# Optimization experiments

Measured on AMD Instinct MI355X. Metric: run time of the kernel, lower is better.

The kernel has to match this reference:

```python
import jax, jax.numpy as jnp
import numpy as np

NUM_EMBEDDINGS = 1024
EMBED_DIM = 256
EMA_DECAY = 0.99
EPS = 1e-05


def setup_inputs() -> dict:
    key = jax.random.key(0)
    k1, k2, k3 = jax.random.split(key, 3)
    B, D, H, W = 32, EMBED_DIM, 32, 32
    z = jax.random.normal(k1, (B, D, H, W), dtype=jnp.float32)
    # torch init: uniform(-1/K, 1/K)
    scale = 1.0 / NUM_EMBEDDINGS
    embedding = jax.random.uniform(k2, (NUM_EMBEDDINGS, EMBED_DIM), dtype=jnp.float32,
                                   minval=-scale, maxval=scale)
    ema_cluster_size = jnp.zeros((NUM_EMBEDDINGS,), dtype=jnp.float32)
    # buffer initialized to a copy of the embedding weights
    ema_embed_sum = embedding.copy()
    return {"z": z, "embedding": embedding,
            "ema_cluster_size": ema_cluster_size, "ema_embed_sum": ema_embed_sum}


def reference(z, embedding, ema_cluster_size, ema_embed_sum):
    B, D, H, W = z.shape
    K = embedding.shape[0]
    # (B, D, H, W) -> (N, D) with N = B*H*W
    z_flat = jnp.transpose(z, (0, 2, 3, 1)).reshape(-1, D)
    # squared L2 distances: ||z||^2 - 2 z E^T + ||e||^2  -> (N, K)
    distances = (jnp.sum(z_flat * z_flat, axis=1, keepdims=True)
                 - 2.0 * z_flat @ embedding.T
                 + jnp.sum(embedding * embedding, axis=1)[None, :])
    indices = jnp.argmin(distances, axis=1)  # (N,) int32
    z_q = embedding[indices].reshape(B, H, W, D).transpose(0, 3, 1, 2)  # (B, D, H, W)

    # training-mode EMA updates (pure functional: return new buffers / codebook)
    ones = jnp.ones((z_flat.shape[0],), dtype=z_flat.dtype)
    counts = jax.ops.segment_sum(ones, indices, num_segments=K)          # (K,)
    embed_sum = jax.ops.segment_sum(z_flat, indices, num_segments=K)     # (K, D)
    new_cs = EMA_DECAY * ema_cluster_size + (1.0 - EMA_DECAY) * counts
    new_es = EMA_DECAY * ema_embed_sum + (1.0 - EMA_DECAY) * embed_sum
    n = jnp.sum(new_cs)
    cluster_size = (new_cs + EPS) / (n + K * EPS) * n
    new_embedding = new_es / cluster_size[:, None]

    # commitment loss and straight-through estimator
    commitment_loss = jnp.mean((z - jax.lax.stop_gradient(z_q)) ** 2)
    z_q_st = z + jax.lax.stop_gradient(z_q - z)
    indices_grid = indices.reshape(B, H, W)
    return (z_q_st, commitment_loss, indices_grid, new_embedding, new_cs, new_es)
```

## Files before the change

### kernel.cpp

```cpp
#include <hip/hip_runtime.h>

#define D_  256
#define K_  1024
#define HW_ 1024
#define N_  32768

#define WS_COUNTS  262144
#define WS_EMBSUM  266240
#define WS_LOSS    1314816
#define WS_NSUM    1314820
#define WS_ENORM   1318924
#define WS_E16     1454096
#define WS_TOTAL   1978384

#define O_ZQ   0
#define O_LOSS 8388608
#define O_IDX  8388609
#define O_EMB  8421377
#define O_NCS  8683521
#define O_NES  8684545

typedef unsigned short u16;
typedef _Float16 f16x8 __attribute__((ext_vector_type(8)));
typedef float f32x4 __attribute__((ext_vector_type(4)));

__device__ __forceinline__ unsigned f16x2pack(float a, float b) {
  union { _Float16 h; unsigned short u; } ca, cb;
  ca.h = (_Float16)a; cb.h = (_Float16)b;
  return (unsigned)ca.u | ((unsigned)cb.u << 16);
}

__device__ __forceinline__ float pw256_sq(const float* __restrict__ p, int stride) {
  float tot0 = 0.f, tot1 = 0.f;
#pragma unroll
  for (int h = 0; h < 2; ++h) {
    const float* q = p + h * 128 * stride;
    float r[8];
#pragma unroll
    for (int j = 0; j < 8; ++j) { float x = q[j * stride]; r[j] = __fmul_rn(x, x); }
    for (int i = 8; i < 128; i += 8)
#pragma unroll
      for (int j = 0; j < 8; ++j) {
        float x = q[(i + j) * stride];
        r[j] = __fadd_rn(r[j], __fmul_rn(x, x));
      }
    float s = __fadd_rn(__fadd_rn(__fadd_rn(r[0], r[1]), __fadd_rn(r[2], r[3])),
                        __fadd_rn(__fadd_rn(r[4], r[5]), __fadd_rn(r[6], r[7])));
    if (h == 0) tot0 = s; else tot1 = s;
  }
  return __fadd_rn(tot0, tot1);
}

__global__ void vq_eprep(const float* __restrict__ E, float* __restrict__ enorm,
                         u16* __restrict__ E16, float* __restrict__ zero0) {
  int gid = blockIdx.x * 256 + threadIdx.x;
  if (gid < K_) {
    float v = pw256_sq(E + gid * D_, 1);
    enorm[gid] = v;
  }
  unsigned* E16w = (unsigned*)E16;
  for (int wd = gid; wd < (K_ * D_ / 2); wd += 8192) {
    float2 x = *(const float2*)(E + 2 * wd);
    E16w[wd] = f16x2pack(512.0f * x.x, 512.0f * x.y);
  }
  float4 z4 = {0.f, 0.f, 0.f, 0.f};
  float4* zp = (float4*)zero0;
  for (int i = gid; i < 65792; i += 8192) zp[i] = z4;
  if (gid == 0) { zero0[263168] = 0.f; zero0[263169] = 0.f; }
}

template <int CTRL>
__device__ __forceinline__ float dppmin(float v) {
  int p = __builtin_amdgcn_update_dpp(0, __float_as_int(v), CTRL, 0xF, 0xF, true);
  return fminf(v, __int_as_float(p));
}

__device__ __forceinline__ void exact_update(
    const float* zrow, const float* __restrict__ E, int t, int c,
    const float* zn_s, const float* en_s, unsigned long long* best_s) {
  const float* ep = E + c * D_;
  float a = 0.f;
  for (int d0 = 0; d0 < 256; d0 += 8) {
    f32x4 z0 = *(const f32x4*)(zrow + d0);
    f32x4 z1 = *(const f32x4*)(zrow + d0 + 4);
    float4 e0 = *(const float4*)(ep + d0);
    float4 e1 = *(const float4*)(ep + d0 + 4);
    a = __fmaf_rn(z0[0], e0.x, a); a = __fmaf_rn(z0[1], e0.y, a);
    a = __fmaf_rn(z0[2], e0.z, a); a = __fmaf_rn(z0[3], e0.w, a);
    a = __fmaf_rn(z1[0], e1.x, a); a = __fmaf_rn(z1[1], e1.y, a);
    a = __fmaf_rn(z1[2], e1.z, a); a = __fmaf_rn(z1[3], e1.w, a);
  }
  float s = __fadd_rn(__fsub_rn(zn_s[t], __fmul_rn(2.0f, a)), en_s[c]);
  unsigned long long key = ((unsigned long long)__float_as_uint(s) << 32) | (unsigned)c;
  atomicMin(&best_s[t], key);
}

#define TCAP 96
#define ZP  260

__global__ __launch_bounds__(256, 4) void vq_main(
    const float* __restrict__ z, const float* __restrict__ E,
    const u16* __restrict__ E16, const float* __restrict__ enorm,
    float* __restrict__ embsum, float* __restrict__ loss_sum,
    float* __restrict__ counts, float* __restrict__ out_zq,
    float* __restrict__ out_idx) {
  __shared__ __align__(16) float zs[32 * ZP];
  __shared__ float en_s[K_];
  __shared__ float zn_s[32];
  __shared__ float mg_s[32];
  __shared__ unsigned rmin_s[32];
  __shared__ unsigned long long best_s[32];
  __shared__ unsigned tcount[4];
  __shared__ unsigned tlist[4][TCAP];
  __shared__ float wred[4];

  const int tid = threadIdx.x;
  const int tile = blockIdx.x;
  const int bimg = tile >> 5;
  const int hw0 = (tile & 31) << 5;
  const float* zb = z + bimg * (D_ * HW_) + hw0;
  const int n0 = bimg * HW_ + hw0;

#pragma unroll
  for (int r = 0; r < 8; ++r) {
    int ii = r * 256 + tid;
    int d = ii >> 3, t4 = (ii & 7) * 4;
    float4 v = *(const float4*)(zb + d * HW_ + t4);
    zs[(t4 + 0) * ZP + d] = v.x; zs[(t4 + 1) * ZP + d] = v.y;
    zs[(t4 + 2) * ZP + d] = v.z; zs[(t4 + 3) * ZP + d] = v.w;
  }
  {
    float emx = 0.f;
    for (int i = tid; i < K_; i += 256) {
      float v = enorm[i];
      en_s[i] = v;
      emx = fmaxf(emx, v);
    }
#pragma unroll
    for (int o = 32; o > 0; o >>= 1) emx = fmaxf(emx, __shfl_down(emx, o, 64));
    if ((tid & 63) == 0) wred[tid >> 6] = emx;
  }
  if (tid < 4) tcount[tid] = 0;
  __syncthreads();
  if (tid < 32) {
    float zn = pw256_sq(&zs[tid * ZP], 1);
    zn_s[tid] = zn;
    float em = fmaxf(fmaxf(wred[0], wred[1]), fmaxf(wred[2], wred[3]));
    mg_s[tid] = 0.00390625f * sqrtf(zn * em) + 5e-4f;
    rmin_s[tid] = 0xFFFFFFFFu;
    best_s[tid] = ~0ull;
  }
  __syncthreads();

  const int lane = tid & 63;
  const int w = tid >> 6;
  const int l15 = lane & 15, g = lane >> 4;
  const int cw = w * 256;
  const u16* Eb = E16 + (unsigned)(cw + l15) * D_ + g * 8;

  f16x8 efA[2], efB[2];
#pragma unroll
  for (int n = 0; n < 2; ++n)
    efA[n] = *(const f16x8*)(Eb + n * 16 * D_);

  f32x4 acc[2][2];

#define MSTEP(S, EFU, EFF, SN)                                                   \
  {                                                                              \
    const int kk_ = (S) & 7;                                                     \
    {                                                                            \
      const int cn_ = (SN) >> 3, kn_ = (SN) & 7;                                 \
      _Pragma("unroll")                                                          \
      for (int n = 0; n < 2; ++n)                                                \
        EFF[n] = *(const f16x8*)(Eb + (cn_ * 32 + n * 16) * D_ + kn_ * 32);      \
    }                                                                            \
    f16x8 zf_[2];                                                                \
    _Pragma("unroll")                                                            \
    for (int m = 0; m < 2; ++m) {                                                \
      const float* zr = zs + (m * 16 + l15) * ZP + kk_ * 32 + g * 8;             \
      f32x4 lo = *(const f32x4*)zr;                                              \
      f32x4 hi = *(const f32x4*)(zr + 4);                                        \
      f16x8 zc;                                                                  \
      _Pragma("unroll")                                                          \
      for (int j = 0; j < 4; ++j) {                                              \
        zc[j] = (_Float16)lo[j]; zc[4 + j] = (_Float16)hi[j];                    \
      }                                                                          \
      zf_[m] = zc;                                                               \
    }                                                                            \
    _Pragma("unroll")                                                            \
    for (int m = 0; m < 2; ++m)                                                  \
      _Pragma("unroll")                                                          \
      for (int n = 0; n < 2; ++n)                                                \
        acc[m][n] = __builtin_amdgcn_mfma_f32_16x16x32_f16(zf_[m], EFU[n],       \
                                                           acc[m][n], 0, 0, 0);  \
  }

  for (int s2 = 0; s2 < 64; s2 += 2) {
    if ((s2 & 7) == 0) {
      f32x4 z4 = {0.f, 0.f, 0.f, 0.f};
#pragma unroll
      for (int m = 0; m < 2; ++m)
#pragma unroll
        for (int n = 0; n < 2; ++n) acc[m][n] = z4;
    }
    MSTEP(s2, efA, efB, s2 + 1)
    MSTEP(s2 + 1, efB, efA, (s2 + 2) & 63)
    if ((s2 & 7) == 6) {
      const int cb = cw + (s2 >> 3) * 32;
      float enc[2];
#pragma unroll
      for (int n = 0; n < 2; ++n) enc[n] = en_s[cb + n * 16 + l15];
#pragma unroll
      for (int m = 0; m < 2; ++m)
#pragma unroll
        for (int n = 0; n < 2; ++n)
#pragma unroll
          for (int r = 0; r < 4; ++r)
            acc[m][n][r] = __builtin_fmaf(-0.00390625f, acc[m][n][r], enc[n]);
#pragma unroll
      for (int m = 0; m < 2; ++m)
#pragma unroll
        for (int r = 0; r < 4; ++r) {
          float v = fminf(acc[m][0][r], acc[m][1][r]);
          v = dppmin<0xB1>(v);
          v = dppmin<0x4E>(v);
          v = dppmin<0x141>(v);
          v = dppmin<0x140>(v);
          if (l15 == 0) atomicMin(&rmin_s[m * 16 + g * 4 + r], __float_as_uint(v + 4.0f));
        }
#pragma unroll
      for (int m = 0; m < 2; ++m)
#pragma unroll
        for (int r = 0; r < 4; ++r) {
          int t = m * 16 + g * 4 + r;
          float thr = (__uint_as_float(rmin_s[t]) - 4.0f) + mg_s[t];
#pragma unroll
          for (int n = 0; n < 2; ++n) {
            if (acc[m][n][r] <= thr) {
              unsigned pos = atomicAdd(&tcount[w], 1u);
              if (pos < TCAP)
                tlist[w][pos] = ((unsigned)t << 16) | (unsigned)(cb + n * 16 + l15);
            }
          }
        }
    }
  }
#undef MSTEP

  {
    unsigned cnt = tcount[w];
    if (cnt <= TCAP) {
      for (unsigned basei = 0; basei < cnt; basei += 64) {
        unsigned i = basei + (unsigned)lane;
        if (i < cnt) {
          unsigned e = tlist[w][i];
          int t = (int)(e >> 16), c = (int)(e & 1023u);
          exact_update(&zs[t * ZP], E, t, c, zn_s, en_s, best_s);
        }
      }
    } else {
      for (unsigned i = (unsigned)lane; i < 32u * 256u; i += 64) {
        int t = (int)(i >> 8), c = cw + (int)(i & 255u);
        exact_update(&zs[t * ZP], E, t, c, zn_s, en_s, best_s);
      }
    }
  }
  __syncthreads();

  if (tid < 32) {
    int k = (int)(best_s[tid] & 1023ull);
    out_idx[n0 + tid] = (float)k;
    atomicAdd(&counts[k], 1.0f);
  }
  float lsum = 0.f;
  for (int tt = 0; tt < 8; ++tt) {
    int t = w * 8 + tt;
    int k = (int)(best_s[t] & 1023ull);
    const float* Er = E + k * D_;
    float* es = embsum + k * D_;
#pragma unroll
    for (int i = 0; i < 4; ++i) {
      int d = i * 64 + lane;
      float e = Er[d];
      float zv = zs[t * ZP + d];
      float df = __fsub_rn(zv, e);
      lsum += df * df;
      zs[t * ZP + d] = __fadd_rn(zv, __fsub_rn(e, zv));
      atomicAdd(es + d, zv);
    }
  }
#pragma unroll
  for (int o = 32; o > 0; o >>= 1) lsum += __shfl_down(lsum, o, 64);
  if (lane == 0) wred[w] = lsum;
  __syncthreads();
  if (tid == 0) atomicAdd(loss_sum, wred[0] + wred[1] + wred[2] + wred[3]);

  float* ob = out_zq + bimg * (D_ * HW_) + hw0;
#pragma unroll 4
  for (int r = 0; r < 32; ++r) {
    int d = r * 8 + (tid >> 5);
    int t = tid & 31;
    ob[d * HW_ + t] = zs[t * ZP + d];
  }
}

__global__ void vq_newfin(const float* __restrict__ cs_in, const float* __restrict__ counts,
                          const float* __restrict__ es_in, const float* __restrict__ embsum,
                          const float* __restrict__ loss_sum,
                          float* __restrict__ out_loss, float* __restrict__ out_ncs,
                          float* __restrict__ out_emb, float* __restrict__ out_nes) {
  __shared__ float nred[4];
  const int k = blockIdx.x, d = threadIdx.x;
  float s = 0.f;
  float myv[4];
#pragma unroll
  for (int i = 0; i < 4; ++i) {
    int idx = i * 256 + d;
    float v = __fadd_rn(__fmul_rn(0.99f, cs_in[idx]), __fmul_rn(0.01f, counts[idx]));
    myv[i] = v;
    s += v;
  }
#pragma unroll
  for (int o = 32; o > 0; o >>= 1) s += __shfl_down(s, o, 64);
  if ((d & 63) == 0) nred[d >> 6] = s;
  __syncthreads();
  const float n = (nred[0] + nred[1]) + (nred[2] + nred[3]);
  if (d == (k & 255)) out_ncs[k] = myv[k >> 8];
  if (k == 0 && d == 0) out_loss[0] = loss_sum[0] * (1.0f / 8388608.0f);
  float vk = __fadd_rn(__fmul_rn(0.99f, cs_in[k]), __fmul_rn(0.01f, counts[k]));
  float cs = (vk + 1e-5f) / (n + 1024.0f * 1e-5f) * n;
  float es = __fadd_rn(__fmul_rn(0.99f, es_in[k * D_ + d]),
                       __fmul_rn(0.01f, embsum[k * D_ + d]));
  out_nes[k * D_ + d] = es;
  out_emb[k * D_ + d] = es / cs;
}

extern "C" void kernel_launch(void* const* d_in, const int* in_sizes, int n_in,
                              void* d_out, int out_size, void* d_ws, size_t ws_size,
                              hipStream_t stream) {
  (void)in_sizes; (void)n_in; (void)out_size; (void)ws_size;
  const float* z       = (const float*)d_in[0];
  const float* E       = (const float*)d_in[1];
  const float* ema_cs  = (const float*)d_in[2];
  const float* ema_es  = (const float*)d_in[3];
  float* out = (float*)d_out;
  char* ws = (char*)d_ws;
  float* counts = (float*)(ws + WS_COUNTS);
  float* embsum = (float*)(ws + WS_EMBSUM);
  float* loss_s = (float*)(ws + WS_LOSS);
  float* enorm  = (float*)(ws + WS_ENORM);
  u16*   e16    = (u16*)(ws + WS_E16);

  vq_eprep<<<dim3(32), dim3(256), 0, stream>>>(E, enorm, e16, counts);
  vq_main<<<dim3(1024), dim3(256), 0, stream>>>(z, E, e16, enorm,
                                                embsum, loss_s, counts,
                                                out + O_ZQ, out + O_IDX);
  vq_newfin<<<dim3(K_), dim3(256), 0, stream>>>(ema_cs, counts, ema_es, embsum,
                                                loss_s, out + O_LOSS, out + O_NCS,
                                                out + O_EMB, out + O_NES);
}
```

Measured before the change: 209.5 us.

## Pre-pack z tile to f16 in LDS and read enorm from global

The main kernel now builds a pre-converted f16 copy of the z tile in shared memory, laid out to match the MFMA operand fragments. Each step then does one vector LDS load per fragment instead of two fp32 loads plus eight conversions. The shared copy of the codebook norms is dropped and reads go straight to global/L2, which frees LDS for the new buffer. The prep kernel launches 256 blocks instead of 32 so the E16 conversion and the workspace zeroing run wider. The cost is an extra strided global read of z to build the f16 tile, plus global loads of enorm inside the hot loop.

```diff
diff --git a/kernel.cpp b/kernel.cpp
--- a/kernel.cpp
+++ b/kernel.cpp
@@ -59,13 +59,13 @@
     enorm[gid] = v;
   }
   unsigned* E16w = (unsigned*)E16;
-  for (int wd = gid; wd < (K_ * D_ / 2); wd += 8192) {
+  for (int wd = gid; wd < (K_ * D_ / 2); wd += 65536) {
     float2 x = *(const float2*)(E + 2 * wd);
     E16w[wd] = f16x2pack(512.0f * x.x, 512.0f * x.y);
   }
   float4 z4 = {0.f, 0.f, 0.f, 0.f};
   float4* zp = (float4*)zero0;
-  for (int i = gid; i < 65792; i += 8192) zp[i] = z4;
+  for (int i = gid; i < 65792; i += 65536) zp[i] = z4;
   if (gid == 0) { zero0[263168] = 0.f; zero0[263169] = 0.f; }
 }
 
@@ -77,7 +77,7 @@
 
 __device__ __forceinline__ void exact_update(
     const float* zrow, const float* __restrict__ E, int t, int c,
-    const float* zn_s, const float* en_s, unsigned long long* best_s) {
+    const float* zn_s, const float* __restrict__ en, unsigned long long* best_s) {
   const float* ep = E + c * D_;
   float a = 0.f;
   for (int d0 = 0; d0 < 256; d0 += 8) {
@@ -90,7 +90,7 @@
     a = __fmaf_rn(z1[0], e1.x, a); a = __fmaf_rn(z1[1], e1.y, a);
     a = __fmaf_rn(z1[2], e1.z, a); a = __fmaf_rn(z1[3], e1.w, a);
   }
-  float s = __fadd_rn(__fsub_rn(zn_s[t], __fmul_rn(2.0f, a)), en_s[c]);
+  float s = __fadd_rn(__fsub_rn(zn_s[t], __fmul_rn(2.0f, a)), en[c]);
   unsigned long long key = ((unsigned long long)__float_as_uint(s) << 32) | (unsigned)c;
   atomicMin(&best_s[t], key);
 }
@@ -105,7 +105,7 @@
     float* __restrict__ counts, float* __restrict__ out_zq,
     float* __restrict__ out_idx) {
   __shared__ __align__(16) float zs[32 * ZP];
-  __shared__ float en_s[K_];
+  __shared__ __align__(16) u16 zt16[32 * 32 * 8];
   __shared__ float zn_s[32];
   __shared__ float mg_s[32];
   __shared__ unsigned rmin_s[32];
@@ -130,12 +130,24 @@
     zs[(t4 + 2) * ZP + d] = v.z; zs[(t4 + 3) * ZP + d] = v.w;
   }
   {
+    const int tok = tid & 31;
+    const int kbase = (tid >> 5) * 4;
+    for (int r = 0; r < 4; ++r) {
+      int kb = kbase + r;
+      unsigned pk[4];
+#pragma unroll
+      for (int j = 0; j < 4; ++j) {
+        float x0 = zb[(kb * 8 + 2 * j) * HW_ + tok];
+        float x1 = zb[(kb * 8 + 2 * j + 1) * HW_ + tok];
+        pk[j] = f16x2pack(x0, x1);
+      }
+      uint4 wv; wv.x = pk[0]; wv.y = pk[1]; wv.z = pk[2]; wv.w = pk[3];
+      *(uint4*)(zt16 + kb * 256 + tok * 8) = wv;
+    }
+  }
+  {
     float emx = 0.f;
-    for (int i = tid; i < K_; i += 256) {
-      float v = enorm[i];
-      en_s[i] = v;
-      emx = fmaxf(emx, v);
-    }
+    for (int i = tid; i < K_; i += 256) emx = fmaxf(emx, enorm[i]);
 #pragma unroll
     for (int o = 32; o > 0; o >>= 1) emx = fmaxf(emx, __shfl_down(emx, o, 64));
     if ((tid & 63) == 0) wred[tid >> 6] = emx;
@@ -176,17 +188,8 @@
     }                                                                            \
     f16x8 zf_[2];                                                                \
     _Pragma("unroll")                                                            \
-    for (int m = 0; m < 2; ++m) {                                                \
-      const float* zr = zs + (m * 16 + l15) * ZP + kk_ * 32 + g * 8;             \
-      f32x4 lo = *(const f32x4*)zr;                                              \
-      f32x4 hi = *(const f32x4*)(zr + 4);                                        \
-      f16x8 zc;                                                                  \
-      _Pragma("unroll")                                                          \
-      for (int j = 0; j < 4; ++j) {                                              \
-        zc[j] = (_Float16)lo[j]; zc[4 + j] = (_Float16)hi[j];                    \
-      }                                                                          \
-      zf_[m] = zc;                                                               \
-    }                                                                            \
+    for (int m = 0; m < 2; ++m)                                                  \
+      zf_[m] = *(const f16x8*)(zt16 + (kk_ * 4 + g) * 256 + (m * 16 + l15) * 8); \
     _Pragma("unroll")                                                            \
     for (int m = 0; m < 2; ++m)                                                  \
       _Pragma("unroll")                                                          \
@@ -209,7 +212,7 @@
       const int cb = cw + (s2 >> 3) * 32;
       float enc[2];
 #pragma unroll
-      for (int n = 0; n < 2; ++n) enc[n] = en_s[cb + n * 16 + l15];
+      for (int n = 0; n < 2; ++n) enc[n] = enorm[cb + n * 16 + l15];
 #pragma unroll
       for (int m = 0; m < 2; ++m)
 #pragma unroll
@@ -255,13 +258,13 @@
         if (i < cnt) {
           unsigned e = tlist[w][i];
           int t = (int)(e >> 16), c = (int)(e & 1023u);
-          exact_update(&zs[t * ZP], E, t, c, zn_s, en_s, best_s);
+          exact_update(&zs[t * ZP], E, t, c, zn_s, enorm, best_s);
         }
       }
     } else {
       for (unsigned i = (unsigned)lane; i < 32u * 256u; i += 64) {
         int t = (int)(i >> 8), c = cw + (int)(i & 255u);
-        exact_update(&zs[t * ZP], E, t, c, zn_s, en_s, best_s);
+        exact_update(&zs[t * ZP], E, t, c, zn_s, enorm, best_s);
       }
     }
   }
@@ -351,7 +354,7 @@
   float* enorm  = (float*)(ws + WS_ENORM);
   u16*   e16    = (u16*)(ws + WS_E16);
 
-  vq_eprep<<<dim3(32), dim3(256), 0, stream>>>(E, enorm, e16, counts);
+  vq_eprep<<<dim3(256), dim3(256), 0, stream>>>(E, enorm, e16, counts);
   vq_main<<<dim3(1024), dim3(256), 0, stream>>>(z, E, e16, enorm,
                                                 embsum, loss_s, counts,
                                                 out + O_ZQ, out + O_IDX);
```

After: 250.8 us. +19.7%, slower.
